# Kernel tuning notes

Measured on AMD Instinct MI355X. Metric: run time of the kernel, lower is better.

## Reference

```python
import jax, jax.numpy as jnp
import numpy as np

D_MODEL = 512
D_K = 64
D_V = 128
H = D_MODEL // D_V  # 4 heads (num_head = d_model // d_v per the source)
B, N = 4, 2048


def setup_inputs() -> dict:
    key = jax.random.key(0)
    k0, k1, k2, k3, k4 = jax.random.split(key, 5)
    s = 0.02
    return {
        "input_x": jax.random.normal(k0, (B, N, D_MODEL), jnp.float32),
        "Wq": jax.random.normal(k1, (D_MODEL, H * D_K), jnp.float32) * s,
        "Wk": jax.random.normal(k2, (D_MODEL, H * D_K), jnp.float32) * s,
        "Wv": jax.random.normal(k3, (D_MODEL, D_MODEL), jnp.float32) * s,
        "Wo": jax.random.normal(k4, (D_MODEL, D_MODEL), jnp.float32) * s,
    }


def reference(input_x, Wq, Wk, Wv, Wo):
    b, n, _ = input_x.shape
    # Contiguous per-head slices in the source == a simple reshape here.
    q = (input_x @ Wq).reshape(b, n, H, D_K)   # [B,N,H,dk]
    k = (input_x @ Wk).reshape(b, n, H, D_K)   # [B,N,H,dk]
    v = (input_x @ Wv).reshape(b, n, H, D_V)   # [B,N,H,dv]
    scale = jnp.sqrt(jnp.float32(D_K))
    scores = jnp.einsum('bqhd,bkhd->bhqk', q, k) / scale  # [B,H,N,N]
    # FAITHFUL quirk: the source uses nn.Softmax() with no dim on a 3D
    # (B,N,N) tensor; PyTorch's legacy dim inference picks dim=0 (batch).
    attn = jax.nn.softmax(scores, axis=0)
    out = jnp.einsum('bhqk,bkhd->bqhd', attn, v).reshape(b, n, H * D_V)
    return out @ Wo
```

## Files before the change

### kernel.cpp

```cpp
#include <hip/hip_runtime.h>
#include <hip/hip_bf16.h>


typedef __attribute__((ext_vector_type(8))) short short8;
typedef __attribute__((ext_vector_type(4))) float floatx4;
typedef unsigned short u16;
typedef unsigned int u32;

#define MFMA16(a, b, c) __builtin_amdgcn_mfma_f32_16x16x32_bf16((a), (b), (c), 0, 0, 0)

__device__ __forceinline__ u16 f2bf(float f) {
    union { float f; unsigned u; } v; v.f = f;
    unsigned r = v.u + 0x7fffu + ((v.u >> 16) & 1u);
    return (u16)(r >> 16);
}

__device__ __forceinline__ float bf2f(u16 b) {
    union { unsigned u; float f; } v; v.u = ((u32)b) << 16;
    return v.f;
}

__device__ __forceinline__ u32 pk2bf(float a, float b) {
#if __has_builtin(__builtin_amdgcn_cvt_pk_bf16_f32)
    typedef __attribute__((ext_vector_type(2))) __bf16 bf16x2;
    union { bf16x2 v; u32 u; } c;
    c.v = __builtin_amdgcn_cvt_pk_bf16_f32(a, b);
    return c.u;
#else
    return (u32)f2bf(a) | ((u32)f2bf(b) << 16);
#endif
}

__device__ __forceinline__ float ex2(float x) {
#if __has_builtin(__builtin_amdgcn_exp2f)
    return __builtin_amdgcn_exp2f(x);
#else
    return exp2f(x);
#endif
}

__device__ __forceinline__ void gload_lds16(const u16* g, u16* l) {
    __builtin_amdgcn_global_load_lds(
        (const __attribute__((address_space(1))) void*)(const void*)g,
        (__attribute__((address_space(3))) void*)(void*)l, 16, 0, 0);
}

__global__ __launch_bounds__(256) void prep_all_kernel(
    const float* __restrict__ x, u16* __restrict__ xb,
    const float* __restrict__ Wq, const float* __restrict__ Wk,
    const float* __restrict__ Wv, const float* __restrict__ Wo,
    u16* __restrict__ WallT, u16* __restrict__ WoT) {
    const int bid = blockIdx.x;
    const int tid = threadIdx.x;
    if (bid < 4096) {
        int i = bid * 256 + tid;
        float4 v = ((const float4*)x)[i];
        ushort4 o;
        o.x = f2bf(v.x); o.y = f2bf(v.y); o.z = f2bf(v.z); o.w = f2bf(v.w);
        ((ushort4*)xb)[i] = o;
        return;
    }
    __shared__ u16 lds[64 * 80];
    const int t = bid - 4096;
    const int k0 = (t & 7) * 64;
    const int n0 = (t >> 3) * 64;
    const float* src; int ld, coff; float scale = 1.0f;
    u16* dst;
    if (n0 < 256)       { src = Wq; ld = 256; coff = n0;        dst = WallT + (size_t)n0 * 512; scale = 0.18033688011f; }
    else if (n0 < 512)  { src = Wk; ld = 256; coff = n0 - 256;  dst = WallT + (size_t)n0 * 512; }
    else if (n0 < 1024) { src = Wv; ld = 512; coff = n0 - 512;  dst = WallT + (size_t)n0 * 512; }
    else                { src = Wo; ld = 512; coff = n0 - 1024; dst = WoT + (size_t)(n0 - 1024) * 512; }
#pragma unroll
    for (int p = 0; p < 4; p++) {
        int r  = (tid >> 4) + p * 16;
        int c4 = (tid & 15) * 4;
        float4 v = *(const float4*)&src[(size_t)(k0 + r) * ld + coff + c4];
        lds[(c4 + 0) * 80 + r] = f2bf(v.x * scale);
        lds[(c4 + 1) * 80 + r] = f2bf(v.y * scale);
        lds[(c4 + 2) * 80 + r] = f2bf(v.z * scale);
        lds[(c4 + 3) * 80 + r] = f2bf(v.w * scale);
    }
    __syncthreads();
#pragma unroll
    for (int p = 0; p < 2; p++) {
        int nn = (tid >> 3) + p * 32;
        int kk = (tid & 7) * 8;
        *(short8*)&dst[(size_t)nn * 512 + k0 + kk] = *(const short8*)&lds[nn * 80 + kk];
    }
}

__global__ __launch_bounds__(512) void gemm_qkv_kernel(
    const u16* __restrict__ A, const u16* __restrict__ BT,
    u16* __restrict__ Qp, u16* __restrict__ Kp, u16* __restrict__ Vp,
    int Kdim) {
    __shared__ u16 sm[16896];
    u16* Asl = sm;
    u16* Bsl = sm + 8192;
    const int tid = threadIdx.x;
    const int bid0 = blockIdx.y * 8 + blockIdx.x;
    const int xcd = bid0 & 7, jj = bid0 >> 3;
    const int mbase = (xcd * 8 + (jj >> 3)) * 128;
    const int nbase = (jj & 7) * 128;
    const int wave = tid >> 6, lane = tid & 63;
    const int wm = wave >> 2, wn = wave & 3;
    const int lq = lane & 15, quad = lane >> 4;

    const int scol = ((lane & 7) ^ (lane >> 3)) * 8;
    const u16* gA = A + (size_t)(mbase + wave * 16 + (lane >> 3)) * Kdim + scol;
    const u16* gB = BT + (size_t)(nbase + wave * 16 + (lane >> 3)) * Kdim + scol;
    u16* lA = &Asl[(wave * 16) * 64];
    u16* lB = &Bsl[(wave * 16) * 64];

    const floatx4 z4 = {0.f, 0.f, 0.f, 0.f};
    floatx4 acc[4][2];
#pragma unroll
    for (int i = 0; i < 4; i++)
#pragma unroll
        for (int j = 0; j < 2; j++) acc[i][j] = z4;

    const int nk = Kdim >> 6;
    for (int kk = 0; kk < nk; kk++) {
        const int kb = kk << 6;
        if (kk) __syncthreads();
#pragma unroll
        for (int i = 0; i < 2; i++) {
            gload_lds16(gA + kb + (size_t)(i * 8) * Kdim, lA + (i * 8) * 64);
            gload_lds16(gB + kb + (size_t)(i * 8) * Kdim, lB + (i * 8) * 64);
        }
        __syncthreads();
#pragma unroll
        for (int ki = 0; ki < 2; ki++) {
            short8 af[4], bf[2];
#pragma unroll
            for (int mi = 0; mi < 4; mi++)
                af[mi] = *(const short8*)&Asl[(wm * 64 + mi * 16 + lq) * 64 +
                                              (((ki * 4 + quad) ^ (lq & 7)) * 8)];
#pragma unroll
            for (int ni = 0; ni < 2; ni++)
                bf[ni] = *(const short8*)&Bsl[(wn * 32 + ni * 16 + lq) * 64 +
                                              (((ki * 4 + quad) ^ (lq & 7)) * 8)];
#pragma unroll
            for (int mi = 0; mi < 4; mi++)
#pragma unroll
                for (int ni = 0; ni < 2; ni++)
                    acc[mi][ni] = MFMA16(af[mi], bf[ni], acc[mi][ni]);
        }
    }
    __syncthreads();
    const bool vtile = (nbase >= 512);
#pragma unroll
    for (int mi = 0; mi < 4; mi++)
#pragma unroll
        for (int ni = 0; ni < 2; ni++) {
            int cl = wn * 32 + ni * 16 + lq;
#pragma unroll
            for (int r = 0; r < 4; r++) {
                int rl = wm * 64 + mi * 16 + quad * 4 + r;
                if (vtile) sm[cl * 132 + rl] = f2bf(acc[mi][ni][r]);
                else       sm[rl * 132 + cl] = f2bf(acc[mi][ni][r]);
            }
        }
    __syncthreads();
    const int b = mbase >> 11;
    const int keyb = mbase & 2047;
    if (nbase < 256) {
        const int hq = nbase >> 6;
        const int qs_base = keyb >> 4;
#pragma unroll
        for (int t = 0; t < 4; t++) {
            int l = wave * 4 + t;
            int qs2 = l >> 2, h2 = (l >> 1) & 1, ki = l & 1;
            int qd = lane >> 4, lqq = lane & 15;
            short8 v = *(const short8*)&sm[(qs2 * 16 + lqq) * 132 + h2 * 64 + ki * 32 + qd * 8];
            int h = hq + h2;
            size_t base = ((size_t)(((b * 4 + h) * 128 + (qs_base + qs2)) * 2 + ki) * 64 + lane) << 3;
            *(short8*)&Qp[base] = v;
        }
    } else if (nbase < 512) {
        const int hb = (nbase - 256) >> 6;
        const int ktb = keyb >> 6;
#pragma unroll
        for (int t = 0; t < 4; t++) {
            int l = wave * 4 + t;
            int kt2 = l >> 4, hf = (l >> 3) & 1, nj = (l >> 2) & 1;
            int h2 = (l >> 1) & 1, ki = l & 1;
            int quadk = lane >> 4, lqk = lane & 15;
            short8 v = *(const short8*)&sm[(kt2 * 64 + hf * 32 + lqk * 2 + nj) * 132 +
                                           h2 * 64 + ki * 32 + quadk * 8];
            int h = hb + h2;
            size_t base = ((size_t)(((((b * 4 + h) * 32 + (ktb + kt2)) * 2 + hf) * 2 + nj)
                                    * 2 + ki) * 64 + lane) << 3;
            *(short8*)&Kp[base] = v;
        }
    } else {
        const int h = (nbase - 512) >> 7;
        const int ktb = keyb >> 6;
#pragma unroll
        for (int t = 0; t < 4; t++) {
            int l = wave * 4 + t;
            int kt2 = l >> 4, hf = (l >> 3) & 1, niv = (l >> 1) & 3, wv = l & 1;
            int quadv = lane >> 4, lqv = lane & 15;
            short8 v = *(const short8*)&sm[(hf * 64 + niv * 16 + lqv) * 132 +
                                           kt2 * 64 + wv * 32 + quadv * 8];
            size_t base = ((size_t)(((((b * 4 + h) * 32 + (ktb + kt2)) * 2 + hf) * 4 + niv)
                                    * 2 + wv) * 64 + lane) << 3;
            *(short8*)&Vp[base] = v;
        }
    }
}

__global__ __launch_bounds__(512) void gemm_out_kernel(
    const u16* __restrict__ A, const u16* __restrict__ BT,
    float* __restrict__ Cf, int Kdim, int ldc) {
    __shared__ u16 Asl[64 * 64];
    __shared__ u16 Bsl[128 * 64];
    const int tid = threadIdx.x;
    const int bid0 = blockIdx.y * 4 + blockIdx.x;
    const int xcd = bid0 & 7, jj = bid0 >> 3;
    const int mbase = (xcd * 16 + (jj >> 2)) * 64;
    const int nbase = (jj & 3) * 128;
    const int wave = tid >> 6, lane = tid & 63;
    const int wm = wave >> 2, wn = wave & 3;
    const int lq = lane & 15, quad = lane >> 4;
    const size_t S = (size_t)8192 * 512;

    const u16* gA = A + (size_t)(mbase + wave * 8 + (lane >> 3)) * Kdim + (lane & 7) * 8;
    const u16* gB = BT + (size_t)(nbase + wave * 16 + (lane >> 3)) * Kdim +
                    (((lane & 7) ^ (lane >> 3)) * 8);
    u16* lAw = &Asl[(wave * 8 + (lane >> 3)) * 64 + (((lane & 7) ^ (lane >> 3)) * 8)];
    u16* lB = &Bsl[(wave * 16) * 64];

    const floatx4 z4 = {0.f, 0.f, 0.f, 0.f};
    floatx4 acc[2][2];
#pragma unroll
    for (int i = 0; i < 2; i++)
#pragma unroll
        for (int j = 0; j < 2; j++) acc[i][j] = z4;

    const int nk = Kdim >> 6;
    for (int kk = 0; kk < nk; kk++) {
        const int kb = kk << 6;
        short8 p0 = *(const short8*)(gA + kb);
        short8 p1 = *(const short8*)(gA + kb + S);
        if (kk) __syncthreads();
        gload_lds16(gB + kb, lB);
        gload_lds16(gB + kb + (size_t)8 * Kdim, lB + 8 * 64);
        short8 o;
#pragma unroll
        for (int j2 = 0; j2 < 8; j2++) {
            float s = bf2f((u16)p0[j2]) + bf2f((u16)p1[j2]);
            o[j2] = (short)f2bf(s);
        }
        *(short8*)lAw = o;
        __syncthreads();
#pragma unroll
        for (int ki = 0; ki < 2; ki++) {
            short8 af[2], bf[2];
#pragma unroll
            for (int mi = 0; mi < 2; mi++)
                af[mi] = *(const short8*)&Asl[(wm * 32 + mi * 16 + lq) * 64 +
                                              (((ki * 4 + quad) ^ (lq & 7)) * 8)];
#pragma unroll
            for (int ni = 0; ni < 2; ni++)
                bf[ni] = *(const short8*)&Bsl[(wn * 32 + ni * 16 + lq) * 64 +
                                              (((ki * 4 + quad) ^ (lq & 7)) * 8)];
#pragma unroll
            for (int mi = 0; mi < 2; mi++)
#pragma unroll
                for (int ni = 0; ni < 2; ni++)
                    acc[mi][ni] = MFMA16(af[mi], bf[ni], acc[mi][ni]);
        }
    }
#pragma unroll
    for (int mi = 0; mi < 2; mi++)
#pragma unroll
        for (int ni = 0; ni < 2; ni++)
#pragma unroll
            for (int r = 0; r < 4; r++)
                Cf[(size_t)(mbase + wm * 32 + mi * 16 + quad * 4 + r) * ldc +
                   (nbase + wn * 32 + ni * 16 + lq)] = acc[mi][ni][r];
}

__global__ __launch_bounds__(512) void attn_kernel(const u16* __restrict__ Qp,
                                                   const u16* __restrict__ Kp,
                                                   const u16* __restrict__ Vp,
                                                   u16* __restrict__ Pp) {
    __shared__ u16 pl[2 * 4 * 4096];
    const int bx = blockIdx.x;
    const int h = bx & 3;
    const int ck = (bx >> 2) & 1;
    const int qt = bx >> 3;
    const int tid = threadIdx.x;
    const int wave = tid >> 6, lane = tid & 63;
    const int mi = wave & 1;
    const int half = (wave >> 1) & 1;
    const int ktq = wave >> 2;
    const int dq = wave;
    const int half_v = dq >> 2, ni_v = dq & 3;
    const int lq = lane & 15, quad = lane >> 4;
    const int qs = qt * 2 + mi;

    short8 aq[4][2];
#pragma unroll
    for (int b = 0; b < 4; b++)
#pragma unroll
        for (int ki = 0; ki < 2; ki++)
            aq[b][ki] = *(const short8*)&Qp[
                ((size_t)((((b * 4 + h) * 128 + qs) * 2 + ki) * 64 + lane) << 3)];

    const floatx4 z4 = {0.f, 0.f, 0.f, 0.f};
    floatx4 oacc[4][2];
#pragma unroll
    for (int b = 0; b < 4; b++)
#pragma unroll
        for (int m2 = 0; m2 < 2; m2++) oacc[b][m2] = z4;

    const int ckb = ck * 16;
    for (int it = 0; it < 8; it++) {
        const int kt = ckb + it * 2 + ktq;
        u16* plb = &pl[(((it & 1) * 2 + ktq) * 2 + mi) * 4096];
        floatx4 s[4][2];
#pragma unroll
        for (int b = 0; b < 4; b++) {
            const u16* kb = Kp +
                ((size_t)((((b * 4 + h) * 32 + kt) * 2 + half) * 2) << 10) +
                lane * 8;
#pragma unroll
            for (int nj = 0; nj < 2; nj++) {
                s[b][nj] = z4;
#pragma unroll
                for (int ki = 0; ki < 2; ki++)
                    s[b][nj] = MFMA16(aq[b][ki],
                                      *(const short8*)(kb + (nj * 2 + ki) * 512),
                                      s[b][nj]);
            }
        }
        short8 vf[2][4][2];
#pragma unroll
        for (int kq = 0; kq < 2; kq++) {
            const int ktv = ckb + it * 2 + kq;
#pragma unroll
            for (int b = 0; b < 4; b++) {
                const u16* vb = Vp +
                    ((size_t)(((((b * 4 + h) * 32 + ktv) * 2 + half_v) * 4 + ni_v) * 2) << 9) +
                    lane * 8;
                vf[kq][b][0] = *(const short8*)vb;
                vf[kq][b][1] = *(const short8*)(vb + 512);
            }
        }
#pragma unroll
        for (int r = 0; r < 4; r++) {
            float e0a = ex2(s[0][0][r]), e0b = ex2(s[0][1][r]);
            float e1a = ex2(s[1][0][r]), e1b = ex2(s[1][1][r]);
            float e2a = ex2(s[2][0][r]), e2b = ex2(s[2][1][r]);
            float e3a = ex2(s[3][0][r]), e3b = ex2(s[3][1][r]);
            float ia = __builtin_amdgcn_rcpf(e0a + e1a + e2a + e3a);
            float ib = __builtin_amdgcn_rcpf(e0b + e1b + e2b + e3b);
            int q = quad * 4 + r;
            int col = (half * 32 + 2 * lq) ^ ((q & 7) * 8);
            *(u32*)&plb[(0 * 16 + q) * 64 + col] = pk2bf(e0a * ia, e0b * ib);
            *(u32*)&plb[(1 * 16 + q) * 64 + col] = pk2bf(e1a * ia, e1b * ib);
            *(u32*)&plb[(2 * 16 + q) * 64 + col] = pk2bf(e2a * ia, e2b * ib);
            *(u32*)&plb[(3 * 16 + q) * 64 + col] = pk2bf(e3a * ia, e3b * ib);
        }
        __syncthreads();
        const int sw = (lq & 7) * 8;
        u16* plbase = &pl[(it & 1) * 4 * 4096];
#pragma unroll
        for (int kq = 0; kq < 2; kq++) {
#pragma unroll
            for (int b = 0; b < 4; b++) {
#pragma unroll
                for (int m2 = 0; m2 < 2; m2++) {
                    const u16* pm = plbase + (kq * 2 + m2) * 4096;
                    short8 ap0 = *(const short8*)&pm[(b * 16 + lq) * 64 + ((quad * 8) ^ sw)];
                    short8 ap1 = *(const short8*)&pm[(b * 16 + lq) * 64 + ((32 + quad * 8) ^ sw)];
                    oacc[b][m2] = MFMA16(ap0, vf[kq][b][0], oacc[b][m2]);
                    oacc[b][m2] = MFMA16(ap1, vf[kq][b][1], oacc[b][m2]);
                }
            }
        }
    }
    u16* Pc = Pp + (size_t)ck * (8192 * 512);
#pragma unroll
    for (int b = 0; b < 4; b++)
#pragma unroll
        for (int m2 = 0; m2 < 2; m2++)
#pragma unroll
            for (int r = 0; r < 4; r++)
                Pc[(size_t)(b * 2048 + qt * 32 + m2 * 16 + quad * 4 + r) * 512 +
                   h * 128 + dq * 16 + lq] = f2bf(oacc[b][m2][r]);
}

extern "C" void kernel_launch(void* const* d_in, const int* in_sizes, int n_in,
                              void* d_out, int out_size, void* d_ws, size_t ws_size,
                              hipStream_t stream) {
    const float* x  = (const float*)d_in[0];
    const float* Wq = (const float*)d_in[1];
    const float* Wk = (const float*)d_in[2];
    const float* Wv = (const float*)d_in[3];
    const float* Wo = (const float*)d_in[4];
    float* out = (float*)d_out;

    char* ws = (char*)d_ws;
    u16* Pp    = (u16*)ws;
    u16* Xb    = (u16*)ws;
    u16* WallT = (u16*)(ws + (size_t)8 * 1024 * 1024);
    char* tail = ws + (size_t)32 * 1024 * 1024;
    u16* WoT   = (u16*)tail; tail += (size_t)512 * 512 * 2;
    u16* Qp    = (u16*)tail; tail += (size_t)8192 * 256 * 2;
    u16* Kp    = (u16*)tail; tail += (size_t)8192 * 256 * 2;
    u16* Vp    = (u16*)tail; tail += (size_t)8192 * 512 * 2;

    prep_all_kernel<<<4288, 256, 0, stream>>>(x, Xb, Wq, Wk, Wv, Wo, WallT, WoT);
    gemm_qkv_kernel<<<dim3(8, 64), 512, 0, stream>>>(Xb, WallT, Qp, Kp, Vp, 512);
    attn_kernel<<<512, 512, 0, stream>>>(Qp, Kp, Vp, Pp);
    gemm_out_kernel<<<dim3(4, 128), 512, 0, stream>>>(Pp, WoT, out, 512, 512);
}
```

Baseline: 158.6 us.

## Cut attention kernel registers and LDS to raise occupancy

Reloads the Q fragments from global memory on every iteration and loads the V fragments per kq step after the barrier, instead of holding them in registers across the loop. The LDS probability buffer is reduced from double to single buffering, which adds a second __syncthreads per iteration, and launch bounds now request 6 waves per EU. The goal is more resident blocks to hide latency, paid for with repeated Q loads, an extra barrier, and V loads no longer overlapping the softmax.

```diff
diff --git a/kernel.cpp b/kernel.cpp
--- a/kernel.cpp
+++ b/kernel.cpp
@@ -281,11 +281,11 @@
                    (nbase + wn * 32 + ni * 16 + lq)] = acc[mi][ni][r];
 }
 
-__global__ __launch_bounds__(512) void attn_kernel(const u16* __restrict__ Qp,
-                                                   const u16* __restrict__ Kp,
-                                                   const u16* __restrict__ Vp,
-                                                   u16* __restrict__ Pp) {
-    __shared__ u16 pl[2 * 4 * 4096];
+__global__ __launch_bounds__(512, 6) void attn_kernel(const u16* __restrict__ Qp,
+                                                      const u16* __restrict__ Kp,
+                                                      const u16* __restrict__ Vp,
+                                                      u16* __restrict__ Pp) {
+    __shared__ u16 pl[4 * 4096];
     const int bx = blockIdx.x;
     const int h = bx & 3;
     const int ck = (bx >> 2) & 1;
@@ -300,14 +300,6 @@
     const int lq = lane & 15, quad = lane >> 4;
     const int qs = qt * 2 + mi;
 
-    short8 aq[4][2];
-#pragma unroll
-    for (int b = 0; b < 4; b++)
-#pragma unroll
-        for (int ki = 0; ki < 2; ki++)
-            aq[b][ki] = *(const short8*)&Qp[
-                ((size_t)((((b * 4 + h) * 128 + qs) * 2 + ki) * 64 + lane) << 3)];
-
     const floatx4 z4 = {0.f, 0.f, 0.f, 0.f};
     floatx4 oacc[4][2];
 #pragma unroll
@@ -316,36 +308,23 @@
         for (int m2 = 0; m2 < 2; m2++) oacc[b][m2] = z4;
 
     const int ckb = ck * 16;
+    u16* plb = &pl[(ktq * 2 + mi) * 4096];
     for (int it = 0; it < 8; it++) {
         const int kt = ckb + it * 2 + ktq;
-        u16* plb = &pl[(((it & 1) * 2 + ktq) * 2 + mi) * 4096];
         floatx4 s[4][2];
 #pragma unroll
         for (int b = 0; b < 4; b++) {
+            const u16* qb = Qp + ((size_t)((((b * 4 + h) * 128 + qs) * 2) * 64 + lane) << 3);
+            short8 aq0 = *(const short8*)qb;
+            short8 aq1 = *(const short8*)(qb + 512);
             const u16* kb = Kp +
                 ((size_t)((((b * 4 + h) * 32 + kt) * 2 + half) * 2) << 10) +
                 lane * 8;
 #pragma unroll
             for (int nj = 0; nj < 2; nj++) {
                 s[b][nj] = z4;
-#pragma unroll
-                for (int ki = 0; ki < 2; ki++)
-                    s[b][nj] = MFMA16(aq[b][ki],
-                                      *(const short8*)(kb + (nj * 2 + ki) * 512),
-                                      s[b][nj]);
-            }
-        }
-        short8 vf[2][4][2];
-#pragma unroll
-        for (int kq = 0; kq < 2; kq++) {
-            const int ktv = ckb + it * 2 + kq;
-#pragma unroll
-            for (int b = 0; b < 4; b++) {
-                const u16* vb = Vp +
-                    ((size_t)(((((b * 4 + h) * 32 + ktv) * 2 + half_v) * 4 + ni_v) * 2) << 9) +
-                    lane * 8;
-                vf[kq][b][0] = *(const short8*)vb;
-                vf[kq][b][1] = *(const short8*)(vb + 512);
+                s[b][nj] = MFMA16(aq0, *(const short8*)(kb + (nj * 2 + 0) * 512), s[b][nj]);
+                s[b][nj] = MFMA16(aq1, *(const short8*)(kb + (nj * 2 + 1) * 512), s[b][nj]);
             }
         }
 #pragma unroll
@@ -365,21 +344,31 @@
         }
         __syncthreads();
         const int sw = (lq & 7) * 8;
-        u16* plbase = &pl[(it & 1) * 4 * 4096];
 #pragma unroll
         for (int kq = 0; kq < 2; kq++) {
+            const int ktv = ckb + it * 2 + kq;
+            short8 vf[4][2];
 #pragma unroll
             for (int b = 0; b < 4; b++) {
+                const u16* vb = Vp +
+                    ((size_t)(((((b * 4 + h) * 32 + ktv) * 2 + half_v) * 4 + ni_v) * 2) << 9) +
+                    lane * 8;
+                vf[b][0] = *(const short8*)vb;
+                vf[b][1] = *(const short8*)(vb + 512);
+            }
+#pragma unroll
+            for (int b = 0; b < 4; b++) {
 #pragma unroll
                 for (int m2 = 0; m2 < 2; m2++) {
-                    const u16* pm = plbase + (kq * 2 + m2) * 4096;
+                    const u16* pm = pl + (kq * 2 + m2) * 4096;
                     short8 ap0 = *(const short8*)&pm[(b * 16 + lq) * 64 + ((quad * 8) ^ sw)];
                     short8 ap1 = *(const short8*)&pm[(b * 16 + lq) * 64 + ((32 + quad * 8) ^ sw)];
-                    oacc[b][m2] = MFMA16(ap0, vf[kq][b][0], oacc[b][m2]);
-                    oacc[b][m2] = MFMA16(ap1, vf[kq][b][1], oacc[b][m2]);
+                    oacc[b][m2] = MFMA16(ap0, vf[b][0], oacc[b][m2]);
+                    oacc[b][m2] = MFMA16(ap1, vf[b][1], oacc[b][m2]);
                 }
             }
         }
+        __syncthreads();
     }
     u16* Pc = Pp + (size_t)ck * (8192 * 512);
 #pragma unroll
```

Result: slower. 275.1 us (+73.4%).
